# Kernel tuning notes

Hardware: AMD Instinct MI355X
Metric: run time of the kernel (lower is better)

The kernel has to match this reference:

```python
import jax, jax.numpy as jnp
import numpy as np

B, S, D = 4, 4096, 1024
DK, DV = 64, 64

def setup_inputs() -> dict:
    key = jax.random.key(0)
    ks = jax.random.split(key, 4)
    scale = 1.0 / np.sqrt(D)
    x = jax.random.normal(ks[0], (B, S, D), dtype=jnp.float32)
    Wq = jax.random.normal(ks[1], (DK, D), dtype=jnp.float32) * scale
    Wk = jax.random.normal(ks[2], (DK, D), dtype=jnp.float32) * scale
    Wv = jax.random.normal(ks[3], (DV, D), dtype=jnp.float32) * scale
    bq = jnp.zeros((DK,), jnp.float32)
    bk = jnp.zeros((DK,), jnp.float32)
    bv = jnp.zeros((DV,), jnp.float32)
    return {"x": x, "Wq": Wq, "bq": bq, "Wk": Wk, "bk": bk, "Wv": Wv, "bv": bv}

def reference(x, Wq, bq, Wk, bk, Wv, bv):
    # Linear projections (torch nn.Linear: y = x @ W.T + b)
    Q = jnp.einsum('bsd,kd->bsk', x, Wq) + bq      # [B,S,DK]
    K = jnp.einsum('bsd,kd->bsk', x, Wk) + bk      # [B,S,DK]
    V = jnp.einsum('bsd,vd->bsv', x, Wv) + bv      # [B,S,DV]
    scale = 1.0 / jnp.sqrt(jnp.float32(DK))
    scores = jnp.einsum('bqk,bsk->bqs', Q, K) * scale  # [B,S,S]
    attn = jax.nn.softmax(scores, axis=-1)
    return jnp.einsum('bqs,bsv->bqv', attn, V)     # [B,S,DV]
```

## Files before the change

kernel.cpp:

```cpp
#include <hip/hip_runtime.h>

typedef unsigned int uint;
typedef unsigned short ushort;

#define SQ 4096
#define DMODEL 1024
#define DH 64
#define NQ 16384
#define QSCALE (0.125f * 1.4426950408889634f)

typedef __attribute__((ext_vector_type(4))) float f32x4;
typedef __attribute__((ext_vector_type(8))) short bf16x8;


__device__ __forceinline__ void ld_lds16(const ushort* g, ushort* l) {
    __builtin_amdgcn_global_load_lds(
        (const __attribute__((address_space(1))) void*)g,
        (__attribute__((address_space(3))) void*)l, 16, 0, 0);
}

__device__ __forceinline__ uint pack2trunc(float a, float b) {
#if __has_builtin(__builtin_amdgcn_perm)
    return __builtin_amdgcn_perm(__float_as_uint(b), __float_as_uint(a),
                                 0x07060302u);
#else
    return (__float_as_uint(a) >> 16) | (__float_as_uint(b) & 0xffff0000u);
#endif
}

__device__ __forceinline__ ushort bf16rne(float a) {
    uint ua = __float_as_uint(a);
    return (ushort)((ua + 0x7fffu + ((ua >> 16) & 1u)) >> 16);
}

#if defined(__HIP_DEVICE_COMPILE__)
#define EXP2(x) __ocml_exp2_f32(x)
extern "C" __device__ float __ocml_exp2_f32(float);
#else
#define EXP2(x) exp2f(x)
#endif

__global__ __launch_bounds__(256) void wsplit_kernel(
    const float* __restrict__ Wq, const float* __restrict__ Wk,
    const float* __restrict__ Wv, ushort* __restrict__ Wch)
{
    int r = blockIdx.x;
    int k = threadIdx.x * 4;
    const float* src = (r < 64)  ? (Wq + r * DMODEL)
                     : (r < 128) ? (Wk + (r - 64) * DMODEL)
                     :             (Wv + (r - 128) * DMODEL);
    float4 v = *(const float4*)&src[k];
    ushort h[4] = {bf16rne(v.x), bf16rne(v.y), bf16rne(v.z), bf16rne(v.w)};
    int ch = k >> 6, kl = k & 63;
    int g = kl >> 3;
    int idx = ch * 12288 + r * 64 + ((g ^ (r & 7)) << 3) + (kl & 7);
    *(ushort4*)&Wch[idx] = make_ushort4(h[0], h[1], h[2], h[3]);
}

__global__ __launch_bounds__(256, 2) void proj_kernel(
    const float* __restrict__ x, const ushort* __restrict__ Wch,
    const float* __restrict__ bq, const float* __restrict__ bk,
    const float* __restrict__ bv,
    ushort* __restrict__ Qr, ushort* __restrict__ Kr, ushort* __restrict__ Vr)
{
    __shared__ ushort sm[32768];

    const int tid  = threadIdx.x;
    const int w    = tid >> 6;
    const int l    = tid & 63;
    const int ln   = l & 15;
    const int quad = l >> 4;
    const int r0   = blockIdx.x << 5;
    const int xr   = tid >> 3;
    const int xs   = tid & 7;
    const int xidx = xr * 64 + ((xs ^ (xr & 7)) << 3);

    f32x4 o_[2][3];
    #pragma unroll
    for (int mt = 0; mt < 2; ++mt)
        #pragma unroll
        for (int nt = 0; nt < 3; ++nt) o_[mt][nt] = (f32x4)0.f;

    float4 xa, xb;
    xa = *(const float4*)&x[(r0 + xr) * DMODEL + xs * 8];
    xb = *(const float4*)&x[(r0 + xr) * DMODEL + xs * 8 + 4];
    {
        const ushort* gh = Wch + w * 3072 + l * 8;
        ushort* dh = sm + 8192 + w * 3072;
        #pragma unroll
        for (int i = 0; i < 6; ++i) ld_lds16(gh + i * 512, dh + i * 512);
    }
    {
        float f[8] = {xa.x, xa.y, xa.z, xa.w, xb.x, xb.y, xb.z, xb.w};
        uint hh[4], ll[4];
        #pragma unroll
        for (int n = 0; n < 4; ++n) {
            float a = f[2 * n], b = f[2 * n + 1];
            float la = a - __uint_as_float(__float_as_uint(a) & 0xffff0000u);
            float lb = b - __uint_as_float(__float_as_uint(b) & 0xffff0000u);
            hh[n] = pack2trunc(a, b);
            ll[n] = pack2trunc(la, lb);
        }
        *(uint4*)&sm[xidx]        = make_uint4(hh[0], hh[1], hh[2], hh[3]);
        *(uint4*)&sm[2048 + xidx] = make_uint4(ll[0], ll[1], ll[2], ll[3]);
    }

    for (int ch = 0; ch < 16; ++ch) {
        const int cur = ch & 1, nxt = cur ^ 1;
        __syncthreads();
        if (ch + 1 < 16) {
            xa = *(const float4*)&x[(r0 + xr) * DMODEL + (ch + 1) * 64 + xs * 8];
            xb = *(const float4*)&x[(r0 + xr) * DMODEL + (ch + 1) * 64 + xs * 8 + 4];
            const ushort* gh = Wch + (ch + 1) * 12288 + w * 3072 + l * 8;
            ushort* dh = sm + 8192 + nxt * 12288 + w * 3072;
            #pragma unroll
            for (int i = 0; i < 6; ++i) ld_lds16(gh + i * 512, dh + i * 512);
        }
        const ushort* Xh = sm + cur * 4096;
        const ushort* Xl = Xh + 2048;
        const ushort* Wh = sm + 8192 + cur * 12288;
        #pragma unroll
        for (int kc = 0; kc < 2; ++kc) {
            int gsw = ((kc * 4 + quad) ^ (ln & 7)) << 3;
            bf16x8 xh[2], xl[2], wh[3];
            #pragma unroll
            for (int mt = 0; mt < 2; ++mt) {
                int off = (mt * 16 + ln) * 64 + gsw;
                xh[mt] = *(bf16x8*)&Xh[off];
                xl[mt] = *(bf16x8*)&Xl[off];
            }
            #pragma unroll
            for (int nt = 0; nt < 3; ++nt)
                wh[nt] = *(bf16x8*)&Wh[(w * 48 + nt * 16 + ln) * 64 + gsw];
            #pragma unroll
            for (int mt = 0; mt < 2; ++mt)
                #pragma unroll
                for (int nt = 0; nt < 3; ++nt) {
                    o_[mt][nt] = __builtin_amdgcn_mfma_f32_16x16x32_bf16(
                        xh[mt], wh[nt], o_[mt][nt], 0, 0, 0);
                    o_[mt][nt] = __builtin_amdgcn_mfma_f32_16x16x32_bf16(
                        xl[mt], wh[nt], o_[mt][nt], 0, 0, 0);
                }
        }
        if (ch + 1 < 16) {
            float f[8] = {xa.x, xa.y, xa.z, xa.w, xb.x, xb.y, xb.z, xb.w};
            uint hh[4], ll[4];
            #pragma unroll
            for (int n = 0; n < 4; ++n) {
                float a = f[2 * n], b = f[2 * n + 1];
                float la = a - __uint_as_float(__float_as_uint(a) & 0xffff0000u);
                float lb = b - __uint_as_float(__float_as_uint(b) & 0xffff0000u);
                hh[n] = pack2trunc(a, b);
                ll[n] = pack2trunc(la, lb);
            }
            *(uint4*)&sm[nxt * 4096 + xidx] =
                make_uint4(hh[0], hh[1], hh[2], hh[3]);
            *(uint4*)&sm[nxt * 4096 + 2048 + xidx] =
                make_uint4(ll[0], ll[1], ll[2], ll[3]);
        }
    }

    __syncthreads();
    uint* Oqk = (uint*)sm;
    uint* Ov  = (uint*)sm + 4096;
    #pragma unroll
    for (int nt = 0; nt < 3; ++nt) {
        int col = 16 * (3 * w + nt) + ln;
        float bias, scl;
        if (col < 64)       { bias = bq[col];       scl = QSCALE; }
        else if (col < 128) { bias = bk[col - 64];  scl = 1.f; }
        else                { bias = bv[col - 128]; scl = 1.f; }
        #pragma unroll
        for (int mt = 0; mt < 2; ++mt)
            #pragma unroll
            for (int j = 0; j < 4; ++j) {
                int m = mt * 16 + quad * 4 + j;
                float val = (o_[mt][nt][j] + bias) * scl;
                if (col < 128) Oqk[m * 128 + col] = (uint)bf16rne(val);
                else {
                    int v = col - 128;
                    Ov[v * 32 + (m ^ ((v & 7) << 2))] = (uint)bf16rne(val);
                }
            }
    }
    __syncthreads();
    const int tile_qk = r0 >> 6;
    const int half    = r0 & 32;
    #pragma unroll
    for (int i = 0; i < 4; ++i) {
        int id = i * 256 + tid;
        int m = id >> 5, g = id & 31;
        uint4 e = *(uint4*)&Oqk[m * 128 + g * 4];
        uint2 hh;
        hh.x = e.x | (e.y << 16);
        hh.y = e.z | (e.w << 16);
        int gg = g & 15;
        int row = half + m;
        int idx = tile_qk * 4096 + row * 64 +
                  (((gg >> 1) ^ (m & 7)) << 3) + (gg & 1) * 4;
        if (g < 16) *(uint2*)&Qr[idx] = hh;
        else        *(uint2*)&Kr[idx] = hh;
    }
    const int vt = (r0 >> 12) * 64 + ((r0 & (SQ - 1)) >> 6);
    #pragma unroll
    for (int i = 0; i < 2; ++i) {
        int id = i * 256 + tid;
        int v = id >> 3, gm = id & 7;
        uint4 e = *(uint4*)&Ov[v * 32 + ((gm ^ (v & 7)) << 2)];
        uint2 hh;
        hh.x = e.x | (e.y << 16);
        hh.y = e.z | (e.w << 16);
        int tg = (half >> 3) + (gm >> 1);
        int idx = vt * 4096 + v * 64 + ((tg ^ (v & 7)) << 3) + (gm & 1) * 4;
        *(uint2*)&Vr[idx] = hh;
    }
}

__global__ __launch_bounds__(256, 3) void attn_kernel(
    const ushort* __restrict__ Qr, const ushort* __restrict__ Kr,
    const ushort* __restrict__ Vr,
    float* __restrict__ opart, float* __restrict__ lpart,
    float* __restrict__ out, int ks)
{
    __shared__ ushort As[24576];

    const int tid  = threadIdx.x;
    const int w    = tid >> 6;
    const int l    = tid & 63;
    const int ln   = l & 15;
    const int quad = l >> 4;

    const int bid   = blockIdx.x;
    const int qb    = bid / ks;
    const int c     = bid - qb * ks;
    const int q0    = qb << 7;
    const int b     = q0 >> 12;
    const int chunk = SQ / ks;
    const int tile0 = (b * SQ + c * chunk) >> 6;
    const int vt0   = b * 64 + ((c * chunk) >> 6);
    const int nIter = chunk >> 6;

    {
        const ushort* gq = Qr + (q0 >> 6) * 4096 + w * 2048 + l * 8;
        #pragma unroll
        for (int i = 0; i < 4; ++i)
            ld_lds16(gq + i * 512, As + w * 2048 + i * 512);
    }
    __syncthreads();
    bf16x8 qf[2][2];
    #pragma unroll
    for (int nt = 0; nt < 2; ++nt)
        #pragma unroll
        for (int kc = 0; kc < 2; ++kc) {
            int row = w * 32 + nt * 16 + ln;
            qf[nt][kc] = *(bf16x8*)&As[row * 64 +
                                       (((kc * 4 + quad) ^ (ln & 7)) << 3)];
        }
    __syncthreads();

    {
        int kt = tile0 * 4096 + w * 1024 + l * 8;
        int vt = vt0 * 4096 + w * 1024 + l * 8;
        ld_lds16(Kr + kt,       As + w * 1024);
        ld_lds16(Kr + kt + 512, As + w * 1024 + 512);
        ld_lds16(Vr + vt,       As + 4096 + w * 1024);
        ld_lds16(Vr + vt + 512, As + 4096 + w * 1024 + 512);
    }

    float l_[2] = {0.f, 0.f};
    f32x4 o_[4][2];
    #pragma unroll
    for (int mt = 0; mt < 4; ++mt)
        #pragma unroll
        for (int nt = 0; nt < 2; ++nt) o_[mt][nt] = (f32x4)0.f;

    for (int it = 0; it < nIter; ++it) {
        const int cur = it & 1, nxt = cur ^ 1;
        __syncthreads();
        if (it + 1 < nIter) {
            int kt = (tile0 + it + 1) * 4096 + w * 1024 + l * 8;
            int vt = (vt0 + it + 1) * 4096 + w * 1024 + l * 8;
            ushort* bb = As + nxt * 8192;
            ld_lds16(Kr + kt,       bb + w * 1024);
            ld_lds16(Kr + kt + 512, bb + w * 1024 + 512);
            ld_lds16(Vr + vt,       bb + 4096 + w * 1024);
            ld_lds16(Vr + vt + 512, bb + 4096 + w * 1024 + 512);
        }
        const ushort* Ks = As + cur * 8192;
        const ushort* Vs = Ks + 4096;
        ushort* Pw = As + 16384 + w * 2048;

        f32x4 s_[4][2];
        #pragma unroll
        for (int mt = 0; mt < 4; ++mt)
            #pragma unroll
            for (int nt = 0; nt < 2; ++nt) s_[mt][nt] = (f32x4)0.f;
        #pragma unroll
        for (int kc = 0; kc < 2; ++kc) {
            int gsw = ((kc * 4 + quad) ^ (ln & 7)) << 3;
            bf16x8 kah[4];
            #pragma unroll
            for (int mt = 0; mt < 4; ++mt)
                kah[mt] = *(bf16x8*)&Ks[(mt * 16 + ln) * 64 + gsw];
            #pragma unroll
            for (int mt = 0; mt < 4; ++mt)
                #pragma unroll
                for (int nt = 0; nt < 2; ++nt)
                    s_[mt][nt] = __builtin_amdgcn_mfma_f32_16x16x32_bf16(
                        kah[mt], qf[nt][kc], s_[mt][nt], 0, 0, 0);
        }

        #pragma unroll
        for (int nt = 0; nt < 2; ++nt) {
            #pragma unroll
            for (int mt = 0; mt < 4; ++mt)
                #pragma unroll
                for (int j = 0; j < 4; ++j) {
                    float p = EXP2(s_[mt][nt][j]);
                    s_[mt][nt][j] = p;
                    l_[nt] += p;
                }
            int q = ln + 16 * nt;
            int sw = ln & 7;
            #pragma unroll
            for (int mt = 0; mt < 4; ++mt) {
                uint2 e;
                e.x = pack2trunc(s_[mt][nt][0], s_[mt][nt][1]);
                e.y = pack2trunc(s_[mt][nt][2], s_[mt][nt][3]);
                int g = 2 * mt + (quad >> 1);
                *(uint2*)&Pw[q * 64 + ((g ^ sw) << 3) + (quad & 1) * 4] = e;
            }
        }

        #pragma unroll
        for (int kc = 0; kc < 2; ++kc) {
            int gsw = ((kc * 4 + quad) ^ (ln & 7)) << 3;
            bf16x8 vah[4], pb[2];
            #pragma unroll
            for (int mt = 0; mt < 4; ++mt)
                vah[mt] = *(bf16x8*)&Vs[(mt * 16 + ln) * 64 + gsw];
            #pragma unroll
            for (int nt = 0; nt < 2; ++nt)
                pb[nt] = *(bf16x8*)&Pw[(ln + 16 * nt) * 64 + gsw];
            #pragma unroll
            for (int mt = 0; mt < 4; ++mt)
                #pragma unroll
                for (int nt = 0; nt < 2; ++nt)
                    o_[mt][nt] = __builtin_amdgcn_mfma_f32_16x16x32_bf16(
                        vah[mt], pb[nt], o_[mt][nt], 0, 0, 0);
        }
    }

    #pragma unroll
    for (int nt = 0; nt < 2; ++nt) {
        l_[nt] += __shfl_xor(l_[nt], 16);
        l_[nt] += __shfl_xor(l_[nt], 32);
    }
    __syncthreads();
    float* tr = (float*)(As + w * 4096);
    if (ks == 1) {
        #pragma unroll
        for (int nt = 0; nt < 2; ++nt) {
            float inv = 1.f / l_[nt];
            #pragma unroll
            for (int mt = 0; mt < 4; ++mt) o_[mt][nt] *= inv;
        }
    }
    #pragma unroll
    for (int p = 0; p < 2; ++p) {
        #pragma unroll
        for (int mt = 0; mt < 4; ++mt)
            #pragma unroll
            for (int j = 0; j < 4; ++j)
                tr[(ln * 16 + ((mt * 4 + quad) ^ ln)) * 4 + j] = o_[mt][p][j];
        #pragma unroll
        for (int i2 = 0; i2 < 4; ++i2) {
            int qt = i2 * 4 + quad;
            f32x4 vv = *(f32x4*)&tr[(qt * 16 + (ln ^ qt)) * 4];
            int qg = q0 + w * 32 + p * 16 + qt;
            if (ks == 1) *(f32x4*)&out[qg * DH + ln * 4] = vv;
            else *(f32x4*)&opart[((size_t)c * NQ + qg) * DH + ln * 4] = vv;
        }
    }
    if (ks > 1 && quad == 0) {
        #pragma unroll
        for (int nt = 0; nt < 2; ++nt) {
            int qg = q0 + w * 32 + 16 * nt + ln;
            lpart[c * NQ + qg] = l_[nt];
        }
    }
}

__global__ __launch_bounds__(256) void attn_combine(
    const float* __restrict__ opart, const float* __restrict__ lpart,
    float* __restrict__ out, int ks)
{
    int id = blockIdx.x * 256 + threadIdx.x;
    int q = id >> 4, c4 = id & 15;
    float den = 0.f;
    f32x4 num = (f32x4)0.f;
    for (int c = 0; c < ks; ++c) {
        den += lpart[c * NQ + q];
        num += *(const f32x4*)&opart[((size_t)c * NQ + q) * DH + c4 * 4];
    }
    float inv = 1.f / den;
    *(f32x4*)&out[q * DH + c4 * 4] = num * inv;
}

extern "C" void kernel_launch(void* const* d_in, const int* in_sizes, int n_in,
                              void* d_out, int out_size, void* d_ws, size_t ws_size,
                              hipStream_t stream) {
    const float* x  = (const float*)d_in[0];
    const float* Wq = (const float*)d_in[1];
    const float* bq = (const float*)d_in[2];
    const float* Wk = (const float*)d_in[3];
    const float* bk = (const float*)d_in[4];
    const float* Wv = (const float*)d_in[5];
    const float* bv = (const float*)d_in[6];
    float* out = (float*)d_out;

    const size_t n16 = (size_t)NQ * DH;
    char* p = (char*)d_ws;
    ushort* Qr = (ushort*)p;           p += n16 * 2;
    ushort* Kr = (ushort*)p;           p += n16 * 2;
    ushort* Vr = (ushort*)p;           p += n16 * 2;
    ushort* Wch = (ushort*)p;          p += 192 * 1024 * 2;

    size_t base = (size_t)(p - (char*)d_ws);
    int ks = 8;
    while (ks > 1 &&
           base + (size_t)ks * n16 * 4 + (size_t)ks * NQ * 4 > ws_size)
        ks >>= 1;

    float* opart = (float*)p;          p += (size_t)ks * n16 * 4;
    float* lpart = (float*)p;

    wsplit_kernel<<<192, 256, 0, stream>>>(Wq, Wk, Wv, Wch);
    proj_kernel<<<NQ / 32, 256, 0, stream>>>(x, Wch, bq, bk, bv, Qr, Kr, Vr);
    attn_kernel<<<(NQ / 128) * ks, 256, 0, stream>>>(
        Qr, Kr, Vr, opart, lpart, out, ks);
    if (ks > 1)
        attn_combine<<<(NQ * 16) / 256, 256, 0, stream>>>(opart, lpart, out, ks);
}
```

Before: 159.5 us.

## Store split-K partial outputs in bf16 and load Q fragments directly from global

Partial attention outputs written by the split attention kernel are now rounded to bf16 (RNE) instead of fp32, halving the write and re-read traffic between attn_kernel and attn_combine. Q fragments are loaded straight from global memory into registers, dropping the LDS staging round trip and two barriers at kernel start. The epilogue transpose uses a separate LDS region so the barrier before it can be removed. The bf16 partials lose precision in the combined output, and the workspace sizing may now allow a larger split count.

Result: no change. 158.1 us, median of 2 (-0.9%).

```diff
diff --git a/kernel.cpp b/kernel.cpp
--- a/kernel.cpp
+++ b/kernel.cpp
@@ -31,6 +31,14 @@
 __device__ __forceinline__ ushort bf16rne(float a) {
     uint ua = __float_as_uint(a);
     return (ushort)((ua + 0x7fffu + ((ua >> 16) & 1u)) >> 16);
+}
+
+__device__ __forceinline__ uint bfpack_rne(float a, float b) {
+    uint ua = __float_as_uint(a);
+    ua = (ua + 0x7fffu + ((ua >> 16) & 1u)) >> 16;
+    uint ub = __float_as_uint(b);
+    ub = (ub + 0x7fffu + ((ub >> 16) & 1u)) & 0xffff0000u;
+    return ua | ub;
 }
 
 #if defined(__HIP_DEVICE_COMPILE__)
@@ -219,7 +227,7 @@
 __global__ __launch_bounds__(256, 3) void attn_kernel(
     const ushort* __restrict__ Qr, const ushort* __restrict__ Kr,
     const ushort* __restrict__ Vr,
-    float* __restrict__ opart, float* __restrict__ lpart,
+    ushort* __restrict__ opart, float* __restrict__ lpart,
     float* __restrict__ out, int ks)
 {
     __shared__ ushort As[24576];
@@ -241,30 +249,26 @@
     const int nIter = chunk >> 6;
 
     {
-        const ushort* gq = Qr + (q0 >> 6) * 4096 + w * 2048 + l * 8;
-        #pragma unroll
-        for (int i = 0; i < 4; ++i)
-            ld_lds16(gq + i * 512, As + w * 2048 + i * 512);
-    }
-    __syncthreads();
-    bf16x8 qf[2][2];
-    #pragma unroll
-    for (int nt = 0; nt < 2; ++nt)
-        #pragma unroll
-        for (int kc = 0; kc < 2; ++kc) {
-            int row = w * 32 + nt * 16 + ln;
-            qf[nt][kc] = *(bf16x8*)&As[row * 64 +
-                                       (((kc * 4 + quad) ^ (ln & 7)) << 3)];
-        }
-    __syncthreads();
-
-    {
         int kt = tile0 * 4096 + w * 1024 + l * 8;
         int vt = vt0 * 4096 + w * 1024 + l * 8;
         ld_lds16(Kr + kt,       As + w * 1024);
         ld_lds16(Kr + kt + 512, As + w * 1024 + 512);
         ld_lds16(Vr + vt,       As + 4096 + w * 1024);
         ld_lds16(Vr + vt + 512, As + 4096 + w * 1024 + 512);
+    }
+
+    bf16x8 qf[2][2];
+    {
+        const ushort* Qbase = Qr + (q0 >> 6) * 4096;
+        #pragma unroll
+        for (int nt = 0; nt < 2; ++nt)
+            #pragma unroll
+            for (int kc = 0; kc < 2; ++kc) {
+                int row = w * 32 + nt * 16 + ln;
+                int off = (row >> 6) * 4096 + (row & 63) * 64 +
+                          (((kc * 4 + quad) ^ (ln & 7)) << 3);
+                qf[nt][kc] = *(const bf16x8*)&Qbase[off];
+            }
     }
 
     float l_[2] = {0.f, 0.f};
@@ -356,8 +360,7 @@
         l_[nt] += __shfl_xor(l_[nt], 16);
         l_[nt] += __shfl_xor(l_[nt], 32);
     }
-    __syncthreads();
-    float* tr = (float*)(As + w * 4096);
+    float* tr = (float*)(As + 16384 + w * 2048);
     if (ks == 1) {
         #pragma unroll
         for (int nt = 0; nt < 2; ++nt) {
@@ -378,8 +381,14 @@
             int qt = i2 * 4 + quad;
             f32x4 vv = *(f32x4*)&tr[(qt * 16 + (ln ^ qt)) * 4];
             int qg = q0 + w * 32 + p * 16 + qt;
-            if (ks == 1) *(f32x4*)&out[qg * DH + ln * 4] = vv;
-            else *(f32x4*)&opart[((size_t)c * NQ + qg) * DH + ln * 4] = vv;
+            if (ks == 1) {
+                *(f32x4*)&out[qg * DH + ln * 4] = vv;
+            } else {
+                uint2 e;
+                e.x = bfpack_rne(vv[0], vv[1]);
+                e.y = bfpack_rne(vv[2], vv[3]);
+                *(uint2*)&opart[((size_t)c * NQ + qg) * DH + ln * 4] = e;
+            }
         }
     }
     if (ks > 1 && quad == 0) {
@@ -392,7 +401,7 @@
 }
 
 __global__ __launch_bounds__(256) void attn_combine(
-    const float* __restrict__ opart, const float* __restrict__ lpart,
+    const ushort* __restrict__ opart, const float* __restrict__ lpart,
     float* __restrict__ out, int ks)
 {
     int id = blockIdx.x * 256 + threadIdx.x;
@@ -401,7 +410,11 @@
     f32x4 num = (f32x4)0.f;
     for (int c = 0; c < ks; ++c) {
         den += lpart[c * NQ + q];
-        num += *(const f32x4*)&opart[((size_t)c * NQ + q) * DH + c4 * 4];
+        ushort4 u = *(const ushort4*)&opart[((size_t)c * NQ + q) * DH + c4 * 4];
+        num[0] += __uint_as_float((uint)u.x << 16);
+        num[1] += __uint_as_float((uint)u.y << 16);
+        num[2] += __uint_as_float((uint)u.z << 16);
+        num[3] += __uint_as_float((uint)u.w << 16);
     }
     float inv = 1.f / den;
     *(f32x4*)&out[q * DH + c4 * 4] = num * inv;
@@ -429,10 +442,10 @@
     size_t base = (size_t)(p - (char*)d_ws);
     int ks = 8;
     while (ks > 1 &&
-           base + (size_t)ks * n16 * 4 + (size_t)ks * NQ * 4 > ws_size)
+           base + (size_t)ks * n16 * 2 + (size_t)ks * NQ * 4 > ws_size)
         ks >>= 1;
 
-    float* opart = (float*)p;          p += (size_t)ks * n16 * 4;
+    ushort* opart = (ushort*)p;        p += (size_t)ks * n16 * 2;
     float* lpart = (float*)p;
 
     wsplit_kernel<<<192, 256, 0, stream>>>(Wq, Wk, Wv, Wch);
```
